# Kernel tuning notes

Measured on AMD Instinct MI355X. Metric: run time of the kernel, lower is better.

The kernel has to match this reference:

```python
import jax, jax.numpy as jnp
import numpy as np

S, B, E, H, DFF = 1024, 8, 1024, 16, 4096
D = E // H
EPS = 1e-5


def _layernorm(x, g, b):
    m = jnp.mean(x, axis=-1, keepdims=True)
    v = jnp.mean(jnp.square(x - m), axis=-1, keepdims=True)
    return (x - m) * jax.lax.rsqrt(v + EPS) * g + b


def setup_inputs() -> dict:
    key = jax.random.key(0)
    ks = jax.random.split(key, 6)
    return {
        "src": jax.random.normal(ks[0], (S, B, E), jnp.float32),
        "in_proj_w": jax.random.normal(ks[1], (3 * E, E), jnp.float32) * (E ** -0.5),
        "in_proj_b": jnp.zeros((3 * E,), jnp.float32),
        "out_w": jax.random.normal(ks[2], (E, E), jnp.float32) * (E ** -0.5),
        "out_b": jnp.zeros((E,), jnp.float32),
        "ln1_g": jnp.ones((E,), jnp.float32),
        "ln1_b": jnp.zeros((E,), jnp.float32),
        "ln2_g": jnp.ones((E,), jnp.float32),
        "ln2_b": jnp.zeros((E,), jnp.float32),
        "w1": jax.random.normal(ks[3], (DFF, E), jnp.float32) * (E ** -0.5),
        "b1": jnp.zeros((DFF,), jnp.float32),
        "w2": jax.random.normal(ks[4], (E, DFF), jnp.float32) * (DFF ** -0.5),
        "b2": jnp.zeros((E,), jnp.float32),
    }


def reference(src, in_proj_w, in_proj_b, out_w, out_b, ln1_g, ln1_b, ln2_g, ln2_b, w1, b1, w2, b2):
    # src: (S, B, E). Packed in-projection: qkv = src @ W^T + b, split into q,k,v.
    qkv = src @ in_proj_w.T + in_proj_b          # (S, B, 3E)
    q, k, v = jnp.split(qkv, 3, axis=-1)
    q = q.reshape(S, B, H, D)
    k = k.reshape(S, B, H, D)
    v = v.reshape(S, B, H, D)
    # Torch scales q by 1/sqrt(head_dim) before the bmm.
    scores = jnp.einsum("sbhd,tbhd->bhst", q * (D ** -0.5), k)   # (B, H, S, S)
    attn = jax.nn.softmax(scores, axis=-1)
    ctx = jnp.einsum("bhst,tbhd->sbhd", attn, v).reshape(S, B, E)
    attn_out = ctx @ out_w.T + out_b
    # Post-norm encoder layer (norm_first=False), dropout=0.
    x = _layernorm(src + attn_out, ln1_g, ln1_b)
    ff = jax.nn.relu(x @ w1.T + b1) @ w2.T + b2
    return _layernorm(x + ff, ln2_g, ln2_b)
```

## Files before the change

### kernel.cpp

```cpp
#include <hip/hip_runtime.h>

#define S_LEN 1024
#define BATCH 8
#define EMB   1024
#define NH    16
#define HD    64
#define FFD   4096
#define ROWS  (S_LEN*BATCH)

typedef __attribute__((ext_vector_type(8))) short  short8;
typedef __attribute__((ext_vector_type(4))) float  float4v;
typedef __attribute__((ext_vector_type(4))) unsigned int uint4v;

struct alignas(8) us4 { unsigned short x, y, z, w; };

__device__ __forceinline__ unsigned short f2bf(float f) {
    unsigned int u = __float_as_uint(f);
    u += 0x7fffu + ((u >> 16) & 1u);
    return (unsigned short)(u >> 16);
}
__device__ __forceinline__ float bf2f(unsigned short b) {
    return __uint_as_float((unsigned int)b << 16);
}
__device__ __forceinline__ unsigned int cvtpk_bf16(float lo, float hi) {
    unsigned int r;
    asm("v_cvt_pk_bf16_f32 %0, %1, %2" : "=v"(r) : "v"(lo), "v"(hi));
    return r;
}
__device__ __forceinline__ float exp2v(float x) {
    float r;
    asm("v_exp_f32 %0, %1" : "=v"(r) : "v"(x));
    return r;
}

__device__ __forceinline__ void gload_lds16(const void* g, void* l) {
    __builtin_amdgcn_global_load_lds(
        (const __attribute__((address_space(1))) unsigned int*)g,
        (__attribute__((address_space(3))) unsigned int*)l, 16, 0, 0);
}

__device__ __forceinline__ int swz(int row, int chunk) {
    return (row << 7) + ((chunk ^ (row & 7)) << 4);
}

__device__ __forceinline__ void xcd_decode(int id, int& lx, int& ly) {
    int k = id & 7, j = id >> 3;
    ly = k * 4 + (j & 3);
    lx = j >> 2;
}

__global__ __launch_bounds__(256) void cast_bf(const float* __restrict__ in,
                                               unsigned short* __restrict__ out,
                                               int n4) {
    int i = blockIdx.x * 256 + threadIdx.x;
    if (i >= n4) return;
    float4 v = ((const float4*)in)[i];
    us4 o = { f2bf(v.x), f2bf(v.y), f2bf(v.z), f2bf(v.w) };
    ((us4*)out)[i] = o;
}

#define QSCALE 0.18033688011112042f
template <int MODE>
__global__ __launch_bounds__(512, 2) void gemm256(const unsigned short* __restrict__ A,
                                                  const unsigned short* __restrict__ Bw,
                                                  const float* __restrict__ bias,
                                                  unsigned short* __restrict__ outb,
                                                  int M, int N, int K) {
    __shared__ char lds[131072];
    const int tid = threadIdx.x, lane = tid & 63, w = tid >> 6;
    const int wr = w >> 2, wc = w & 3;
    int lx, ly;
    xcd_decode(blockIdx.x, lx, ly);
    const int m0 = ly * 256, n0 = lx * 256;
    const int nt = K >> 6;

    size_t baseA[2], baseB[2];
    int ldsOff[2];
#pragma unroll
    for (int q = 0; q < 2; ++q) {
        int ci = q * 512 + tid;
        int row = ci >> 3;
        int c = (ci & 7) ^ (row & 7);
        baseA[q] = (size_t)(m0 + row) * K + c * 8;
        baseB[q] = (size_t)(n0 + row) * K + c * 8;
        ldsOff[q] = ci * 16;
    }

    auto stage = [&](int kt, int which) {
        int ktc = kt < nt ? kt : 0;
        int slot = kt & 1;
        if (which < 2) {
#pragma unroll
            for (int q = 0; q < 2; ++q)
                gload_lds16(A + baseA[q] + (size_t)which * 128 * K + (size_t)ktc * 64,
                            lds + slot * 32768 + which * 16384 + ldsOff[q]);
        } else {
            int h = which - 2;
#pragma unroll
            for (int q = 0; q < 2; ++q)
                gload_lds16(Bw + baseB[q] + (size_t)h * 128 * K + (size_t)ktc * 64,
                            lds + 65536 + slot * 32768 + h * 16384 + ldsOff[q]);
        }
    };

    auto rdA = [&](int slot, int mh, int i, int mk) -> short8 {
        int arow = wr * 128 + mh * 64 + i * 16 + (lane & 15);
        return *(const short8*)(lds + slot * 32768 + swz(arow, mk * 4 + (lane >> 4)));
    };
    auto rdB = [&](int slot, int nh, int j, int mk) -> short8 {
        int brow = wc * 64 + nh * 32 + j * 16 + (lane & 15);
        return *(const short8*)(lds + 65536 + slot * 32768 + swz(brow, mk * 4 + (lane >> 4)));
    };

    float4v acc[8][4];
#pragma unroll
    for (int i = 0; i < 8; ++i)
#pragma unroll
        for (int j = 0; j < 4; ++j) acc[i][j] = (float4v){0.f, 0.f, 0.f, 0.f};

    short8 a[4][2], b[2][2][2];

    stage(0, 0); stage(0, 1); stage(0, 2); stage(0, 3);
    stage(1, 0);
    asm volatile("s_waitcnt vmcnt(2)" ::: "memory");
    __builtin_amdgcn_s_barrier();

#define MFMA16(MH, NH)                                                          \
    __builtin_amdgcn_s_setprio(1);                                              \
    _Pragma("unroll")                                                           \
    for (int i = 0; i < 4; ++i)                                                 \
        _Pragma("unroll")                                                       \
        for (int j = 0; j < 2; ++j) {                                           \
            acc[(MH)*4+i][(NH)*2+j] = __builtin_amdgcn_mfma_f32_16x16x32_bf16(  \
                a[i][0], b[NH][j][0], acc[(MH)*4+i][(NH)*2+j], 0, 0, 0);        \
            acc[(MH)*4+i][(NH)*2+j] = __builtin_amdgcn_mfma_f32_16x16x32_bf16(  \
                a[i][1], b[NH][j][1], acc[(MH)*4+i][(NH)*2+j], 0, 0, 0);        \
        }                                                                       \
    __builtin_amdgcn_s_setprio(0);

    for (int t = 0; t < nt; ++t) {
        const int slot = t & 1;
#pragma unroll
        for (int i = 0; i < 4; ++i) {
            a[i][0] = rdA(slot, 0, i, 0);
            a[i][1] = rdA(slot, 0, i, 1);
        }
#pragma unroll
        for (int j = 0; j < 2; ++j) {
            b[0][j][0] = rdB(slot, 0, j, 0);
            b[0][j][1] = rdB(slot, 0, j, 1);
        }
        stage(t + 1, 1);
        __builtin_amdgcn_s_barrier();
        asm volatile("s_waitcnt lgkmcnt(0)" ::: "memory");
        __builtin_amdgcn_sched_barrier(0);
        MFMA16(0, 0)
        __builtin_amdgcn_s_barrier();
#pragma unroll
        for (int j = 0; j < 2; ++j) {
            b[1][j][0] = rdB(slot, 1, j, 0);
            b[1][j][1] = rdB(slot, 1, j, 1);
        }
        stage(t + 1, 2);
        __builtin_amdgcn_s_barrier();
        asm volatile("s_waitcnt lgkmcnt(0)" ::: "memory");
        __builtin_amdgcn_sched_barrier(0);
        MFMA16(0, 1)
        __builtin_amdgcn_s_barrier();
#pragma unroll
        for (int i = 0; i < 4; ++i) {
            a[i][0] = rdA(slot, 1, i, 0);
            a[i][1] = rdA(slot, 1, i, 1);
        }
        stage(t + 1, 3);
        __builtin_amdgcn_s_barrier();
        asm volatile("s_waitcnt lgkmcnt(0)" ::: "memory");
        __builtin_amdgcn_sched_barrier(0);
        MFMA16(1, 1)
        __builtin_amdgcn_s_barrier();
        stage(t + 2, 0);
        MFMA16(1, 0)
        asm volatile("s_waitcnt vmcnt(2)" ::: "memory");
        __builtin_amdgcn_s_barrier();
    }
#undef MFMA16
    asm volatile("s_waitcnt vmcnt(0)" ::: "memory");

#pragma unroll
    for (int mi = 0; mi < 8; ++mi) {
#pragma unroll
        for (int nj = 0; nj < 4; ++nj) {
            int col = n0 + wc * 64 + nj * 16 + (lane & 15);
            float bv = bias[col];
#pragma unroll
            for (int r = 0; r < 4; ++r) {
                int row = m0 + wr * 128 + mi * 16 + (lane >> 4) * 4 + r;
                size_t idx = (size_t)row * N + col;
                float v = acc[mi][nj][r] + bv;
                if (MODE == 0) {
                    if (col < EMB) v *= QSCALE;
                    outb[idx] = f2bf(v);
                } else {
                    outb[idx] = f2bf(fmaxf(v, 0.f));
                }
            }
        }
    }
}

template <int MODE>
__global__ __launch_bounds__(512, 2) void gemm256n(const unsigned short* __restrict__ A,
                                                   const unsigned short* __restrict__ Bw,
                                                   const float* __restrict__ bias,
                                                   const float* __restrict__ res,
                                                   const unsigned short* __restrict__ resb,
                                                   float* __restrict__ outf,
                                                   int M, int N, int K) {
    __shared__ char lds[147456];
    const int tid = threadIdx.x, lane = tid & 63, w = tid >> 6;
    const int wr = w >> 1, wc = w & 1;
    int lx, ly;
    xcd_decode(blockIdx.x, lx, ly);
    const int m0 = ly * 256, n0 = lx * 128;
    const int nt = K >> 6;
    const int g = lane >> 4, qs = lane & 15;

    size_t baseA[4], baseB[2];
    int ldsOffA[4], ldsOffB[2];
#pragma unroll
    for (int q = 0; q < 4; ++q) {
        int ci = q * 512 + tid;
        int row = ci >> 3;
        int c = (ci & 7) ^ (row & 7);
        baseA[q] = (size_t)(m0 + row) * K + c * 8;
        ldsOffA[q] = ci * 16;
    }
#pragma unroll
    for (int q = 0; q < 2; ++q) {
        int ci = q * 512 + tid;
        int row = ci >> 3;
        int c = (ci & 7) ^ (row & 7);
        baseB[q] = (size_t)(n0 + row) * K + c * 8;
        ldsOffB[q] = ci * 16;
    }

    auto stage = [&](int kt) {
        int ktc = kt < nt ? kt : 0;
        int slot = kt % 3;
#pragma unroll
        for (int q = 0; q < 4; ++q)
            gload_lds16(A + baseA[q] + (size_t)ktc * 64,
                        lds + slot * 32768 + ldsOffA[q]);
#pragma unroll
        for (int q = 0; q < 2; ++q)
            gload_lds16(Bw + baseB[q] + (size_t)ktc * 64,
                        lds + 98304 + slot * 16384 + ldsOffB[q]);
    };

    auto rdA = [&](int slot, int i, int mk) -> short8 {
        int arow = wr * 64 + i * 16 + qs;
        return *(const short8*)(lds + slot * 32768 + swz(arow, mk * 4 + g));
    };
    auto rdB = [&](int slot, int j, int mk) -> short8 {
        int brow = wc * 64 + j * 16 + qs;
        return *(const short8*)(lds + 98304 + slot * 16384 + swz(brow, mk * 4 + g));
    };

    float4v acc[4][4];
#pragma unroll
    for (int i = 0; i < 4; ++i)
#pragma unroll
        for (int j = 0; j < 4; ++j) acc[i][j] = (float4v){0.f, 0.f, 0.f, 0.f};

    short8 a[4][2], b[4][2];

    stage(0); stage(1);
    asm volatile("s_waitcnt vmcnt(6)" ::: "memory");
    __builtin_amdgcn_s_barrier();

    for (int t = 0; t < nt; ++t) {
        const int slot = t % 3;
#pragma unroll
        for (int i = 0; i < 4; ++i) {
            a[i][0] = rdA(slot, i, 0);
            a[i][1] = rdA(slot, i, 1);
        }
#pragma unroll
        for (int j = 0; j < 4; ++j) {
            b[j][0] = rdB(slot, j, 0);
            b[j][1] = rdB(slot, j, 1);
        }
        stage(t + 2);
        asm volatile("s_waitcnt lgkmcnt(0)" ::: "memory");
        __builtin_amdgcn_sched_barrier(0);
        __builtin_amdgcn_s_setprio(1);
#pragma unroll
        for (int i = 0; i < 4; ++i)
#pragma unroll
            for (int j = 0; j < 4; ++j) {
                acc[i][j] = __builtin_amdgcn_mfma_f32_16x16x32_bf16(
                    a[i][0], b[j][0], acc[i][j], 0, 0, 0);
                acc[i][j] = __builtin_amdgcn_mfma_f32_16x16x32_bf16(
                    a[i][1], b[j][1], acc[i][j], 0, 0, 0);
            }
        __builtin_amdgcn_s_setprio(0);
        asm volatile("s_waitcnt vmcnt(6)" ::: "memory");
        __builtin_amdgcn_s_barrier();
    }
    asm volatile("s_waitcnt vmcnt(0)" ::: "memory");

#pragma unroll
    for (int mi = 0; mi < 4; ++mi) {
#pragma unroll
        for (int j = 0; j < 4; ++j) {
            int col = n0 + wc * 64 + j * 16 + qs;
            float bv = bias[col];
#pragma unroll
            for (int r = 0; r < 4; ++r) {
                int row = m0 + wr * 64 + mi * 16 + g * 4 + r;
                size_t idx = (size_t)row * N + col;
                float v = acc[mi][j][r] + bv;
                if (MODE == 1) outf[idx] = v + res[idx];
                else           outf[idx] = v + bf2f(resb[idx]);
            }
        }
    }
}

__global__ __launch_bounds__(256) void vtrans(const unsigned short* __restrict__ qkv,
                                              unsigned short* __restrict__ vt) {
    const int bh = blockIdx.y, b = bh >> 4, h = bh & 15;
    const int t0 = blockIdx.x * 64;
    const int tid = threadIdx.x;
    __shared__ unsigned short lds[64][72];
#pragma unroll
    for (int rep = 0; rep < 2; ++rep) {
        int slot = rep * 256 + tid;
        int row = slot >> 3, cc = slot & 7;
        const unsigned short* g =
            qkv + ((size_t)(t0 + row) * BATCH + b) * 3072 + 2 * EMB + h * 64 + cc * 8;
        *(uint4v*)&lds[row][cc * 8] = *(const uint4v*)g;
    }
    __syncthreads();
#pragma unroll
    for (int rep = 0; rep < 2; ++rep) {
        int slot = rep * 256 + tid;
        int d = slot >> 3, tc = slot & 7;
        unsigned short tmp[8] __attribute__((aligned(16)));
#pragma unroll
        for (int j = 0; j < 8; ++j) tmp[j] = lds[tc * 8 + j][d];
        unsigned short* g = vt + ((size_t)bh * 64 + d) * S_LEN + t0 + tc * 8;
        *(uint4v*)g = *(const uint4v*)tmp;
    }
}

__global__ __launch_bounds__(256, 6) void attn(const unsigned short* __restrict__ qkv,
                                               const unsigned short* __restrict__ vt,
                                               unsigned short* __restrict__ ctx) {
    __shared__ char Ks[64 * 128];
    __shared__ char Vs[64 * 128];
    __shared__ char QP[64 * 128];
    const int tid = threadIdx.x, lane = tid & 63, w = tid >> 6;
    const int bh = blockIdx.x & 127, b = bh >> 4, h = bh & 15;
    const int s0 = (blockIdx.x >> 7) * 64;
    const int g = lane >> 4, qs = lane & 15;

#pragma unroll
    for (int p = 0; p < 2; ++p) {
        int ci = p * 256 + tid;
        int row = ci >> 3, c = (ci & 7) ^ (row & 7);
        gload_lds16(qkv + ((size_t)(s0 + row) * BATCH + b) * 3072 + h * 64 + c * 8,
                    QP + (p * 256 + w * 64) * 16);
    }
    __syncthreads();

    short8 qa0 = *(const short8*)(QP + swz(w * 16 + qs, 0 * 4 + g));
    short8 qa1 = *(const short8*)(QP + swz(w * 16 + qs, 1 * 4 + g));
    asm volatile("s_waitcnt lgkmcnt(0)" ::: "memory");
    __builtin_amdgcn_sched_barrier(0);
    char* Ps = QP + w * 2048;

    float4v O[4];
#pragma unroll
    for (int df = 0; df < 4; ++df) O[df] = (float4v){0.f, 0.f, 0.f, 0.f};
    float m_s = -1e30f;
    float l_s = 0.f;

    for (int t0 = 0; t0 < S_LEN; t0 += 64) {
        __syncthreads();
#pragma unroll
        for (int p = 0; p < 2; ++p) {
            int ci = p * 256 + tid;
            int row = ci >> 3, c = (ci & 7) ^ (row & 7);
            gload_lds16(qkv + ((size_t)(t0 + row) * BATCH + b) * 3072 + EMB + h * 64 + c * 8,
                        Ks + (p * 256 + w * 64) * 16);
            gload_lds16(vt + ((size_t)bh * 64 + row) * S_LEN + t0 + c * 8,
                        Vs + (p * 256 + w * 64) * 16);
        }
        __syncthreads();

        float4v Sf[4];
#pragma unroll
        for (int tf = 0; tf < 4; ++tf) Sf[tf] = (float4v){0.f, 0.f, 0.f, 0.f};
#pragma unroll
        for (int tf = 0; tf < 4; ++tf) {
            int kr = tf * 16 + qs;
            short8 kb0 = *(const short8*)(Ks + swz(kr, 0 * 4 + g));
            short8 kb1 = *(const short8*)(Ks + swz(kr, 1 * 4 + g));
            Sf[tf] = __builtin_amdgcn_mfma_f32_16x16x32_bf16(kb0, qa0, Sf[tf], 0, 0, 0);
            Sf[tf] = __builtin_amdgcn_mfma_f32_16x16x32_bf16(kb1, qa1, Sf[tf], 0, 0, 0);
        }

        float mx = fmaxf(fmaxf(Sf[0][0], Sf[0][1]), fmaxf(Sf[0][2], Sf[0][3]));
#pragma unroll
        for (int tf = 1; tf < 4; ++tf)
            mx = fmaxf(mx, fmaxf(fmaxf(Sf[tf][0], Sf[tf][1]),
                                 fmaxf(Sf[tf][2], Sf[tf][3])));
        mx = fmaxf(mx, __shfl_xor(mx, 16));
        mx = fmaxf(mx, __shfl_xor(mx, 32));

        if (!__all(mx - m_s <= 8.0f)) {
            float mnew = fmaxf(m_s, mx);
            float alpha = exp2v(m_s - mnew);
            m_s = mnew;
            l_s *= alpha;
#pragma unroll
            for (int r = 0; r < 4; ++r) {
                float ar = __shfl(alpha, 4 * g + r);
#pragma unroll
                for (int df = 0; df < 4; ++df) O[df][r] *= ar;
            }
        }

        float rs = 0.f;
#pragma unroll
        for (int tf = 0; tf < 4; ++tf) {
            float p0 = exp2v(Sf[tf][0] - m_s);
            float p1 = exp2v(Sf[tf][1] - m_s);
            float p2 = exp2v(Sf[tf][2] - m_s);
            float p3 = exp2v(Sf[tf][3] - m_s);
            rs += (p0 + p1) + (p2 + p3);
            uint2 pk = make_uint2(cvtpk_bf16(p0, p1), cvtpk_bf16(p2, p3));
            *(uint2*)(Ps + (qs << 7) +
                      (((2 * tf + (g >> 1)) ^ (qs & 7)) << 4) + ((g & 1) << 3)) = pk;
        }
        rs += __shfl_xor(rs, 16);
        rs += __shfl_xor(rs, 32);
        l_s += rs;

        asm volatile("s_waitcnt lgkmcnt(0)" ::: "memory");
        __builtin_amdgcn_sched_barrier(0);

#pragma unroll
        for (int mk = 0; mk < 2; ++mk) {
            short8 pa = *(const short8*)(Ps + swz(qs, mk * 4 + g));
#pragma unroll
            for (int df = 0; df < 4; ++df) {
                int vr = df * 16 + qs;
                short8 vb = *(const short8*)(Vs + swz(vr, mk * 4 + g));
                O[df] = __builtin_amdgcn_mfma_f32_16x16x32_bf16(pa, vb, O[df], 0, 0, 0);
            }
        }
    }

    float inv = __builtin_amdgcn_rcpf(l_s);
#pragma unroll
    for (int r = 0; r < 4; ++r) {
        float ir = __shfl(inv, 4 * g + r);
#pragma unroll
        for (int df = 0; df < 4; ++df) {
            int srow = s0 + w * 16 + g * 4 + r;
            int d    = df * 16 + qs;
            ctx[((size_t)srow * BATCH + b) * EMB + h * 64 + d] = f2bf(O[df][r] * ir);
        }
    }
}

__global__ __launch_bounds__(256) void ln_ker(const float* __restrict__ y,
                                              const float* __restrict__ g,
                                              const float* __restrict__ bta,
                                              float* __restrict__ xo,
                                              unsigned short* __restrict__ xb) {
    const int row = blockIdx.x, tid = threadIdx.x, lane = tid & 63, w = tid >> 6;
    float4 v = ((const float4*)(y + (size_t)row * EMB))[tid];
    float s = v.x + v.y + v.z + v.w;
    float q = v.x * v.x + v.y * v.y + v.z * v.z + v.w * v.w;
#pragma unroll
    for (int m = 1; m < 64; m <<= 1) {
        s += __shfl_xor(s, m);
        q += __shfl_xor(q, m);
    }
    __shared__ float ps[4], pq[4];
    if (lane == 0) { ps[w] = s; pq[w] = q; }
    __syncthreads();
    s = ps[0] + ps[1] + ps[2] + ps[3];
    q = pq[0] + pq[1] + pq[2] + pq[3];
    float mean = s * (1.f / EMB);
    float var  = q * (1.f / EMB) - mean * mean;
    float rstd = rsqrtf(var + 1e-5f);
    float4 gv = ((const float4*)g)[tid];
    float4 bv = ((const float4*)bta)[tid];
    float4 o;
    o.x = (v.x - mean) * rstd * gv.x + bv.x;
    o.y = (v.y - mean) * rstd * gv.y + bv.y;
    o.z = (v.z - mean) * rstd * gv.z + bv.z;
    o.w = (v.w - mean) * rstd * gv.w + bv.w;
    if (xo) ((float4*)(xo + (size_t)row * EMB))[tid] = o;
    if (xb) {
        us4 ob = { f2bf(o.x), f2bf(o.y), f2bf(o.z), f2bf(o.w) };
        ((us4*)(xb + (size_t)row * EMB))[tid] = ob;
    }
}

extern "C" void kernel_launch(void* const* d_in, const int* in_sizes, int n_in,
                              void* d_out, int out_size, void* d_ws, size_t ws_size,
                              hipStream_t stream) {
    (void)in_sizes; (void)n_in; (void)out_size;
    const float* src       = (const float*)d_in[0];
    const float* in_proj_w = (const float*)d_in[1];
    const float* in_proj_b = (const float*)d_in[2];
    const float* out_w     = (const float*)d_in[3];
    const float* out_b     = (const float*)d_in[4];
    const float* ln1_g     = (const float*)d_in[5];
    const float* ln1_b     = (const float*)d_in[6];
    const float* ln2_g     = (const float*)d_in[7];
    const float* ln2_b     = (const float*)d_in[8];
    const float* w1        = (const float*)d_in[9];
    const float* b1        = (const float*)d_in[10];
    const float* w2        = (const float*)d_in[11];
    const float* b2        = (const float*)d_in[12];

    const size_t MB = 1u << 20;
    if (ws_size < 104 * MB) return;

    char* ws = (char*)d_ws;
    unsigned short* wqkvb = (unsigned short*)(ws);
    unsigned short* wob   = (unsigned short*)(ws + 6 * MB);
    unsigned short* w1b   = (unsigned short*)(ws + 8 * MB);
    unsigned short* w2b   = (unsigned short*)(ws + 16 * MB);
    unsigned short* qkvb  = (unsigned short*)(ws + 24 * MB);
    unsigned short* srcbf = (unsigned short*)(ws + 72 * MB);
    unsigned short* vtb   = (unsigned short*)(ws + 88 * MB);
    unsigned short* ctxb  = (unsigned short*)(ws + 72 * MB);
    unsigned short* xbf   = (unsigned short*)(ws + 24 * MB);
    unsigned short* hb    = (unsigned short*)(ws + 40 * MB);
    float*          yout  = (float*)d_out;

    auto castn = [&](const float* in, unsigned short* out, size_t n) {
        int n4 = (int)(n / 4);
        cast_bf<<<(n4 + 255) / 256, 256, 0, stream>>>(in, out, n4);
    };
    castn(src, srcbf, (size_t)ROWS * EMB);
    castn(in_proj_w, wqkvb, (size_t)3 * EMB * EMB);
    castn(out_w, wob, (size_t)EMB * EMB);
    castn(w1, w1b, (size_t)FFD * EMB);
    castn(w2, w2b, (size_t)EMB * FFD);

    gemm256<0><<<(3 * EMB / 256) * 32, 512, 0, stream>>>(
        srcbf, wqkvb, in_proj_b, qkvb, ROWS, 3 * EMB, EMB);

    vtrans<<<dim3(S_LEN / 64, BATCH * NH), 256, 0, stream>>>(qkvb, vtb);

    attn<<<(S_LEN / 64) * BATCH * NH, 256, 0, stream>>>(qkvb, vtb, ctxb);

    gemm256n<1><<<(EMB / 128) * 32, 512, 0, stream>>>(
        ctxb, wob, out_b, src, nullptr, yout, ROWS, EMB, EMB);

    ln_ker<<<ROWS, 256, 0, stream>>>(yout, ln1_g, ln1_b, nullptr, xbf);

    gemm256<2><<<(FFD / 256) * 32, 512, 0, stream>>>(
        xbf, w1b, b1, hb, ROWS, FFD, EMB);

    gemm256n<3><<<(EMB / 128) * 32, 512, 0, stream>>>(
        hb, w2b, b2, nullptr, xbf, yout, ROWS, EMB, FFD);

    ln_ker<<<ROWS, 256, 0, stream>>>(yout, ln2_g, ln2_b, (float*)d_out, nullptr);
}
```

Baseline: 331.9 us.

## Restructure gemm256 LDS staging into 8 rotating half-tiles with deeper prefetch

```diff
diff --git a/kernel.cpp b/kernel.cpp
--- a/kernel.cpp
+++ b/kernel.cpp
@@ -69,47 +69,44 @@
     __shared__ char lds[131072];
     const int tid = threadIdx.x, lane = tid & 63, w = tid >> 6;
     const int wr = w >> 2, wc = w & 3;
+    const int g = lane >> 4, qs = lane & 15;
     int lx, ly;
     xcd_decode(blockIdx.x, lx, ly);
     const int m0 = ly * 256, n0 = lx * 256;
     const int nt = K >> 6;
 
-    size_t baseA[2], baseB[2];
+    size_t hof[4][2];
     int ldsOff[2];
 #pragma unroll
     for (int q = 0; q < 2; ++q) {
         int ci = q * 512 + tid;
         int row = ci >> 3;
         int c = (ci & 7) ^ (row & 7);
-        baseA[q] = (size_t)(m0 + row) * K + c * 8;
-        baseB[q] = (size_t)(n0 + row) * K + c * 8;
         ldsOff[q] = ci * 16;
-    }
-
-    auto stage = [&](int kt, int which) {
+        hof[0][q] = (size_t)(n0 + row) * K + c * 8;
+        hof[1][q] = (size_t)(n0 + 128 + row) * K + c * 8;
+        hof[2][q] = (size_t)(m0 + row) * K + c * 8;
+        hof[3][q] = (size_t)(m0 + 128 + row) * K + c * 8;
+    }
+
+    auto stageH = [&](int s) {
+        int k = s & 3;
+        int kt = s >> 2;
         int ktc = kt < nt ? kt : 0;
-        int slot = kt & 1;
-        if (which < 2) {
-#pragma unroll
-            for (int q = 0; q < 2; ++q)
-                gload_lds16(A + baseA[q] + (size_t)which * 128 * K + (size_t)ktc * 64,
-                            lds + slot * 32768 + which * 16384 + ldsOff[q]);
-        } else {
-            int h = which - 2;
-#pragma unroll
-            for (int q = 0; q < 2; ++q)
-                gload_lds16(Bw + baseB[q] + (size_t)h * 128 * K + (size_t)ktc * 64,
-                            lds + 65536 + slot * 32768 + h * 16384 + ldsOff[q]);
-        }
-    };
-
-    auto rdA = [&](int slot, int mh, int i, int mk) -> short8 {
-        int arow = wr * 128 + mh * 64 + i * 16 + (lane & 15);
-        return *(const short8*)(lds + slot * 32768 + swz(arow, mk * 4 + (lane >> 4)));
-    };
-    auto rdB = [&](int slot, int nh, int j, int mk) -> short8 {
-        int brow = wc * 64 + nh * 32 + j * 16 + (lane & 15);
-        return *(const short8*)(lds + 65536 + slot * 32768 + swz(brow, mk * 4 + (lane >> 4)));
+        char* dst = lds + ((s & 7) << 14);
+        const unsigned short* src = (k < 2) ? Bw : A;
+#pragma unroll
+        for (int q = 0; q < 2; ++q)
+            gload_lds16(src + hof[k][q] + (size_t)ktc * 64, dst + ldsOff[q]);
+    };
+
+    auto rdA = [&](int par, int ig, int mk) -> short8 {
+        char* half = lds + ((par * 4 + 2 + wr) << 14);
+        return *(const short8*)(half + swz(ig * 16 + qs, mk * 4 + g));
+    };
+    auto rdB = [&](int par, int j, int mk) -> short8 {
+        char* half = lds + ((par * 4 + (wc >> 1)) << 14);
+        return *(const short8*)(half + swz((wc & 1) * 64 + j * 16 + qs, mk * 4 + g));
     };
 
     float4v acc[8][4];
@@ -118,83 +115,75 @@
 #pragma unroll
         for (int j = 0; j < 4; ++j) acc[i][j] = (float4v){0.f, 0.f, 0.f, 0.f};
 
-    short8 a[4][2], b[2][2][2];
-
-    stage(0, 0); stage(0, 1); stage(0, 2); stage(0, 3);
-    stage(1, 0);
-    asm volatile("s_waitcnt vmcnt(2)" ::: "memory");
+    short8 a[4][2], b[4][2];
+
+    stageH(0); stageH(1); stageH(2); stageH(3);
+    stageH(4); stageH(5); stageH(6);
+    asm volatile("s_waitcnt vmcnt(6)" ::: "memory");
     __builtin_amdgcn_s_barrier();
 
-#define MFMA16(MH, NH)                                                          \
+#define CLUSTER(MH, NH)                                                         \
     __builtin_amdgcn_s_setprio(1);                                              \
     _Pragma("unroll")                                                           \
     for (int i = 0; i < 4; ++i)                                                 \
         _Pragma("unroll")                                                       \
-        for (int j = 0; j < 2; ++j) {                                           \
-            acc[(MH)*4+i][(NH)*2+j] = __builtin_amdgcn_mfma_f32_16x16x32_bf16(  \
-                a[i][0], b[NH][j][0], acc[(MH)*4+i][(NH)*2+j], 0, 0, 0);        \
-            acc[(MH)*4+i][(NH)*2+j] = __builtin_amdgcn_mfma_f32_16x16x32_bf16(  \
-                a[i][1], b[NH][j][1], acc[(MH)*4+i][(NH)*2+j], 0, 0, 0);        \
+        for (int jj = 0; jj < 2; ++jj) {                                        \
+            acc[(MH)*4+i][(NH)*2+jj] = __builtin_amdgcn_mfma_f32_16x16x32_bf16( \
+                a[i][0], b[(NH)*2+jj][0], acc[(MH)*4+i][(NH)*2+jj], 0, 0, 0);   \
+            acc[(MH)*4+i][(NH)*2+jj] = __builtin_amdgcn_mfma_f32_16x16x32_bf16( \
+                a[i][1], b[(NH)*2+jj][1], acc[(MH)*4+i][(NH)*2+jj], 0, 0, 0);   \
         }                                                                       \
     __builtin_amdgcn_s_setprio(0);
 
     for (int t = 0; t < nt; ++t) {
-        const int slot = t & 1;
+        const int par = t & 1;
 #pragma unroll
         for (int i = 0; i < 4; ++i) {
-            a[i][0] = rdA(slot, 0, i, 0);
-            a[i][1] = rdA(slot, 0, i, 1);
-        }
-#pragma unroll
-        for (int j = 0; j < 2; ++j) {
-            b[0][j][0] = rdB(slot, 0, j, 0);
-            b[0][j][1] = rdB(slot, 0, j, 1);
-        }
-        stage(t + 1, 1);
+            a[i][0] = rdA(par, i, 0);
+            a[i][1] = rdA(par, i, 1);
+        }
+#pragma unroll
+        for (int j = 0; j < 4; ++j) {
+            b[j][0] = rdB(par, j, 0);
+            b[j][1] = rdB(par, j, 1);
+        }
+        stageH(4 * t + 7);
         __builtin_amdgcn_s_barrier();
         asm volatile("s_waitcnt lgkmcnt(0)" ::: "memory");
         __builtin_amdgcn_sched_barrier(0);
-        MFMA16(0, 0)
-        __builtin_amdgcn_s_barrier();
-#pragma unroll
-        for (int j = 0; j < 2; ++j) {
-            b[1][j][0] = rdB(slot, 1, j, 0);
-            b[1][j][1] = rdB(slot, 1, j, 1);
-        }
-        stage(t + 1, 2);
+        CLUSTER(0, 0)
+        __builtin_amdgcn_s_barrier();
+        stageH(4 * t + 8);
+        CLUSTER(0, 1)
+        __builtin_amdgcn_s_barrier();
+#pragma unroll
+        for (int i = 0; i < 4; ++i) {
+            a[i][0] = rdA(par, 4 + i, 0);
+            a[i][1] = rdA(par, 4 + i, 1);
+        }
+        stageH(4 * t + 9);
         __builtin_amdgcn_s_barrier();
         asm volatile("s_waitcnt lgkmcnt(0)" ::: "memory");
         __builtin_amdgcn_sched_barrier(0);
-        MFMA16(0, 1)
-        __builtin_amdgcn_s_barrier();
-#pragma unroll
-        for (int i = 0; i < 4; ++i) {
-            a[i][0] = rdA(slot, 1, i, 0);
-            a[i][1] = rdA(slot, 1, i, 1);
-        }
-        stage(t + 1, 3);
-        __builtin_amdgcn_s_barrier();
-        asm volatile("s_waitcnt lgkmcnt(0)" ::: "memory");
-        __builtin_amdgcn_sched_barrier(0);
-        MFMA16(1, 1)
-        __builtin_amdgcn_s_barrier();
-        stage(t + 2, 0);
-        MFMA16(1, 0)
-        asm volatile("s_waitcnt vmcnt(2)" ::: "memory");
-        __builtin_amdgcn_s_barrier();
-    }
-#undef MFMA16
+        CLUSTER(1, 0)
+        __builtin_amdgcn_s_barrier();
+        stageH(4 * t + 10);
+        CLUSTER(1, 1)
+        asm volatile("s_waitcnt vmcnt(6)" ::: "memory");
+        __builtin_amdgcn_s_barrier();
+    }
+#undef CLUSTER
     asm volatile("s_waitcnt vmcnt(0)" ::: "memory");
 
 #pragma unroll
     for (int mi = 0; mi < 8; ++mi) {
 #pragma unroll
         for (int nj = 0; nj < 4; ++nj) {
-            int col = n0 + wc * 64 + nj * 16 + (lane & 15);
+            int col = n0 + wc * 64 + nj * 16 + qs;
             float bv = bias[col];
 #pragma unroll
             for (int r = 0; r < 4; ++r) {
-                int row = m0 + wr * 128 + mi * 16 + (lane >> 4) * 4 + r;
+                int row = m0 + wr * 128 + mi * 16 + g * 4 + r;
                 size_t idx = (size_t)row * N + col;
                 float v = acc[mi][nj][r] + bv;
                 if (MODE == 0) {
```

Measured after the change: 333.6 us. No clear change (+0.5%).
